# Optimization experiments

Hardware: AMD Instinct MI355X
Metric: run time of the kernel (lower is better)

The kernel has to match this reference:

```python
import jax, jax.numpy as jnp
import numpy as np

N_HEAD = 8
D_HEAD = 64
HIDDEN = 512
T = 2048
BS = 4
SCALE = D_HEAD ** -0.5


def setup_inputs() -> dict:
    key = jax.random.key(0)
    k1, k2, k3 = jax.random.split(key, 3)
    x = jax.random.normal(k1, (BS, T, HIDDEN), dtype=jnp.float32)
    # torch Linear weight is (out,in); we store as (in,out) for x @ W
    W_qkv = jax.random.normal(k2, (HIDDEN, (2 * N_HEAD + 1) * D_HEAD), dtype=jnp.float32) * 0.02
    W_out = jax.random.normal(k3, (D_HEAD, HIDDEN), dtype=jnp.float32) * 0.02
    return {"x": x, "W_qkv": W_qkv, "W_out": W_out}


def reference(x, W_qkv, W_out):
    bs, t, h = x.shape
    qkv = x @ W_qkv  # (bs, t, (2H+1)*d)
    q, k, v = jnp.split(qkv, [N_HEAD * D_HEAD, 2 * N_HEAD * D_HEAD], axis=-1)
    q = q.reshape(bs, t, N_HEAD, D_HEAD)
    k = k.reshape(bs, t, N_HEAD, D_HEAD)
    # v is shared across heads: (bs, t, d)
    score = jnp.einsum("bqhd,bkhd->bhqk", q, k) * SCALE
    causal = jnp.triu(jnp.full((t, t), -jnp.inf, dtype=score.dtype), 1)
    score = score + causal[None, None, :, :]
    prob = jax.nn.softmax(score, axis=-1)  # (bs, H, t, t)
    attn_vec = jnp.einsum("bhqk,bkd->bhqd", prob, v)  # shared V broadcast over heads
    m_attn_vec = jnp.mean(attn_vec, axis=1)  # head-mean: (bs, t, d)
    out = m_attn_vec @ W_out  # (bs, t, hidden)
    return out, attn_vec
```

## Files before the change

kernel.cpp:

```cpp
#include <hip/hip_runtime.h>
#include <hip/hip_bf16.h>

#define NHEAD  8
#define DHEAD  64
#define HIDDEN 512
#define SEQ_T  2048
#define BATCH  4
#define NQKV   1088
#define QPITCH 1152
#define NT     32
#define NROWS  (BATCH * SEQ_T)
#define NBH    (BATCH * NHEAD)
#define QSC    (0.125f * 1.44269504f)

typedef __attribute__((ext_vector_type(8))) short short8;
typedef __attribute__((ext_vector_type(4))) float f32x4;

__device__ __forceinline__ unsigned short f2bf(float f) {
  unsigned int u = __float_as_uint(f);
  u += 0x7FFFu + ((u >> 16) & 1u);
  return (unsigned short)(u >> 16);
}
__device__ __forceinline__ float bf2f(unsigned short u) {
  return __uint_as_float((unsigned int)u << 16);
}

__device__ __forceinline__ void load_lds16(const unsigned short* g, unsigned short* l) {
  __builtin_amdgcn_global_load_lds((const __attribute__((address_space(1))) void*)g,
                                   (__attribute__((address_space(3))) void*)l, 16, 0, 0);
}

__global__ __launch_bounds__(256) void prep(const float* __restrict__ x,
                                            const float* __restrict__ W,
                                            unsigned short* __restrict__ xb,
                                            unsigned short* __restrict__ Wt) {
  const int bx = blockIdx.x;
  const int tid = threadIdx.x;
  if (bx < 2048) {
    const size_t i0 = ((size_t)bx * 256 + tid) * 8;
    float4 a = *(const float4*)(x + i0);
    float4 b = *(const float4*)(x + i0 + 4);
    ushort4 u0, u1;
    u0.x = f2bf(a.x); u0.y = f2bf(a.y); u0.z = f2bf(a.z); u0.w = f2bf(a.w);
    u1.x = f2bf(b.x); u1.y = f2bf(b.y); u1.z = f2bf(b.z); u1.w = f2bf(b.w);
    *(ushort4*)(xb + i0) = u0;
    *(ushort4*)(xb + i0 + 4) = u1;
    return;
  }
  if (bx >= 2184) {
    const int z = bx - 2184;
    const size_t base = (size_t)NQKV * HIDDEN + ((size_t)z * 256 + tid) * 16;
    uint4 zero = {0u, 0u, 0u, 0u};
    *(uint4*)(Wt + base) = zero;
    *(uint4*)(Wt + base + 8) = zero;
    return;
  }
  const int idx = bx - 2048;
  const int n0 = (idx % 17) * 64;
  const int k0 = (idx / 17) * 64;
  __shared__ float T[64 * 65];
#pragma unroll
  for (int i = 0; i < 4; ++i) {
    int f = tid + i * 256;
    int r = f >> 4;
    int c4 = (f & 15) * 4;
    float4 v = *(const float4*)(W + (size_t)(k0 + r) * NQKV + n0 + c4);
    T[r * 65 + c4 + 0] = v.x;
    T[r * 65 + c4 + 1] = v.y;
    T[r * 65 + c4 + 2] = v.z;
    T[r * 65 + c4 + 3] = v.w;
  }
  __syncthreads();
#pragma unroll
  for (int i = 0; i < 4; ++i) {
    int f = tid + i * 256;
    int n = f >> 4;
    int k4 = (f & 15) * 4;
    ushort4 u;
    u.x = f2bf(T[(k4 + 0) * 65 + n]);
    u.y = f2bf(T[(k4 + 1) * 65 + n]);
    u.z = f2bf(T[(k4 + 2) * 65 + n]);
    u.w = f2bf(T[(k4 + 3) * 65 + n]);
    *(ushort4*)(Wt + (size_t)(n0 + n) * HIDDEN + k0 + k4) = u;
  }
}

__global__ __launch_bounds__(256, 3) void qkv_mfma(const unsigned short* __restrict__ Xb,
                                                   const unsigned short* __restrict__ Wt,
                                                   unsigned short* __restrict__ Y) {
  __shared__ __align__(16) unsigned short As[128 * 64];
  __shared__ __align__(16) unsigned short Bs[128 * 64];
  const int L = blockIdx.x;
  const int slot = L >> 3;
  const int bm = (L & 7) * 8 + (slot & 7);
  const int bn = slot >> 3;
  const int tid = threadIdx.x;
  const int wave = tid >> 6;
  const int lane = tid & 63;
  const int quad = lane >> 4;
  const int l15 = lane & 15;
  const int lrow = lane >> 3;
  const int lchunk = lane & 7;

  const unsigned short* xrow = Xb + (size_t)bm * 128 * HIDDEN;
  const unsigned short* wrow = Wt + (size_t)bn * 128 * HIDDEN;

  f32x4 acc[2][8];
#pragma unroll
  for (int mt = 0; mt < 2; ++mt)
#pragma unroll
    for (int nt = 0; nt < 8; ++nt) acc[mt][nt] = (f32x4){0.f, 0.f, 0.f, 0.f};

  for (int k0 = 0; k0 < HIDDEN; k0 += 64) {
    __syncthreads();
#pragma unroll
    for (int c = 0; c < 4; ++c) {
      int call = wave * 4 + c;
      int m = call * 8 + lrow;
      int clog = lchunk ^ lrow;
      load_lds16(xrow + (size_t)m * HIDDEN + k0 + clog * 8, &As[call * 512]);
      load_lds16(wrow + (size_t)m * HIDDEN + k0 + clog * 8, &Bs[call * 512]);
    }
    __syncthreads();

#pragma unroll
    for (int ks = 0; ks < 2; ++ks) {
      short8 a[2], b[8];
#pragma unroll
      for (int mt = 0; mt < 2; ++mt) {
        int m = wave * 32 + mt * 16 + l15;
        int phys = (ks * 4 + quad) ^ (l15 & 7);
        a[mt] = *(const short8*)&As[m * 64 + phys * 8];
      }
#pragma unroll
      for (int nt = 0; nt < 8; ++nt) {
        int n = nt * 16 + l15;
        int phys = (ks * 4 + quad) ^ (l15 & 7);
        b[nt] = *(const short8*)&Bs[n * 64 + phys * 8];
      }
#pragma unroll
      for (int mt = 0; mt < 2; ++mt)
#pragma unroll
        for (int nt = 0; nt < 8; ++nt)
          acc[mt][nt] = __builtin_amdgcn_mfma_f32_16x16x32_bf16(a[mt], b[nt], acc[mt][nt], 0, 0, 0);
    }
  }

  const float qs = (bn < 4) ? QSC : 1.0f;
#pragma unroll
  for (int mt = 0; mt < 2; ++mt)
#pragma unroll
    for (int r = 0; r < 4; ++r) {
      int row = bm * 128 + wave * 32 + mt * 16 + quad * 4 + r;
#pragma unroll
      for (int nt = 0; nt < 8; ++nt) {
        int col = bn * 128 + nt * 16 + l15;
        Y[(size_t)row * QPITCH + col] = f2bf(acc[mt][nt][r] * qs);
      }
    }
}

__global__ __launch_bounds__(256) void v_transpose(const unsigned short* __restrict__ qkv,
                                                   unsigned short* __restrict__ vt) {
  const int b = blockIdx.x >> 5;
  const int k0 = (blockIdx.x & 31) * 64;
  const int tid = threadIdx.x;
  __shared__ unsigned short Vs[64 * 66];

#pragma unroll
  for (int i = 0; i < 8; ++i) {
    int c = tid + i * 256;
    int row = c >> 5;
    int col2 = c & 31;
    unsigned int v = *(const unsigned int*)(qkv + (size_t)(b * SEQ_T + k0 + row) * QPITCH + 1024 + col2 * 2);
    *(unsigned int*)&Vs[row * 66 + col2 * 2] = v;
  }
  __syncthreads();

#pragma unroll
  for (int i = 0; i < 16; ++i) {
    int f = tid + i * 256;
    int d = f >> 6;
    int n = f & 63;
    int c = (n & 32) | ((n & 4) << 2) | ((n >> 1) & 12) | (n & 3);
    vt[((size_t)b * DHEAD + d) * SEQ_T + k0 + n] = Vs[c * 66 + d];
  }
}

__global__ __launch_bounds__(256, 4) void attn_pass(const unsigned short* __restrict__ qkv,
                                                    const unsigned short* __restrict__ vt,
                                                    unsigned short* __restrict__ pbuf0,
                                                    unsigned short* __restrict__ pbuf1,
                                                    float* __restrict__ lbuf) {
  const int bh = blockIdx.x;
  const int y = blockIdx.y;
  const int qt = 15 - (y >> 1);
  const int kh = y & 1;
  const int b = bh >> 3;
  const int h = bh & 7;
  const int tid = threadIdx.x;
  const int wave = tid >> 6;
  const int lane = tid & 63;
  const int quad = lane >> 4;
  const int l15 = lane & 15;

  __shared__ __align__(16) unsigned short Ks[2][64 * 64];
  __shared__ __align__(16) unsigned short Vts[2][64 * 64];

  const unsigned short* bq = qkv + (size_t)b * SEQ_T * QPITCH;
  const unsigned short* bvt = vt + (size_t)b * DHEAD * SEQ_T;

  const int q0 = qt * 128;
  const int kbeg = kh ? (qt + 1) : 0;
  const int kend = kh ? (2 * qt + 1) : qt;

  short8 aq[2][2];
#pragma unroll
  for (int s = 0; s < 2; ++s) {
    const unsigned short* qp = bq + (size_t)(q0 + s * 64 + wave * 16 + l15) * QPITCH + h * 64 + quad * 8;
    aq[s][0] = *(const short8*)qp;
    aq[s][1] = *(const short8*)(qp + 32);
  }

  f32x4 o[2][4];
#pragma unroll
  for (int s = 0; s < 2; ++s)
#pragma unroll
    for (int t = 0; t < 4; ++t) o[s][t] = (f32x4){0.f, 0.f, 0.f, 0.f};
  float l_part[2] = {0.f, 0.f};

  const int srow = tid >> 3;
  const int sch = (tid & 7) ^ (srow & 7);
  const int ph0 = (quad ^ (l15 & 7)) * 8;

#pragma unroll
  for (int c = 0; c < 2; ++c) {
    load_lds16(bq + (size_t)(kbeg * 64 + c * 32 + srow) * QPITCH + 512 + h * 64 + sch * 8,
               &Ks[0][c * 2048 + wave * 512]);
    load_lds16(bvt + (size_t)(c * 32 + srow) * SEQ_T + kbeg * 64 + sch * 8,
               &Vts[0][c * 2048 + wave * 512]);
  }

  for (int kt = kbeg; kt <= kend; ++kt) {
    const int k0 = kt * 64;
    const int cur = (kt - kbeg) & 1;
    __syncthreads();
    if (kt < kend) {
      const int kn = (kt + 1) * 64;
      const int nxt = cur ^ 1;
#pragma unroll
      for (int c = 0; c < 2; ++c) {
        load_lds16(bq + (size_t)(kn + c * 32 + srow) * QPITCH + 512 + h * 64 + sch * 8,
                   &Ks[nxt][c * 2048 + wave * 512]);
        load_lds16(bvt + (size_t)(c * 32 + srow) * SEQ_T + kn + sch * 8,
                   &Vts[nxt][c * 2048 + wave * 512]);
      }
    }

    const unsigned short* ksb = Ks[cur];
    const unsigned short* vsb = Vts[cur];
    const bool needMask = (k0 + 63) > q0;

    short8 bk[4][2];
#pragma unroll
    for (int t = 0; t < 4; ++t) {
      const unsigned short* kp = &ksb[(l15 + 16 * t) * 64];
      bk[t][0] = *(const short8*)(kp + ph0);
      bk[t][1] = *(const short8*)(kp + (ph0 ^ 32));
    }

    short8 ap[2][2];
#pragma unroll
    for (int s = 0; s < 2; ++s) {
      f32x4 pr[4];
#pragma unroll
      for (int t = 0; t < 4; ++t) {
        f32x4 sv = (f32x4){0.f, 0.f, 0.f, 0.f};
        sv = __builtin_amdgcn_mfma_f32_16x16x32_bf16(bk[t][0], aq[s][0], sv, 0, 0, 0);
        sv = __builtin_amdgcn_mfma_f32_16x16x32_bf16(bk[t][1], aq[s][1], sv, 0, 0, 0);
        pr[t] = sv;
      }
      const int qrow = q0 + s * 64 + wave * 16 + l15;
#pragma unroll
      for (int t = 0; t < 4; ++t)
#pragma unroll
        for (int r = 0; r < 4; ++r) {
          float p = __builtin_amdgcn_exp2f(pr[t][r]);
          if (needMask)
            p = (k0 + 16 * t + 4 * quad + r <= qrow) ? p : 0.f;
          l_part[s] += p;
          pr[t][r] = p;
        }
#pragma unroll
      for (int c = 0; c < 2; ++c) {
        union { unsigned int u[4]; short8 v; } pk;
        pk.u[0] = __builtin_amdgcn_perm(__float_as_uint(pr[2 * c][1]),
                                        __float_as_uint(pr[2 * c][0]), 0x07060302u);
        pk.u[1] = __builtin_amdgcn_perm(__float_as_uint(pr[2 * c][3]),
                                        __float_as_uint(pr[2 * c][2]), 0x07060302u);
        pk.u[2] = __builtin_amdgcn_perm(__float_as_uint(pr[2 * c + 1][1]),
                                        __float_as_uint(pr[2 * c + 1][0]), 0x07060302u);
        pk.u[3] = __builtin_amdgcn_perm(__float_as_uint(pr[2 * c + 1][3]),
                                        __float_as_uint(pr[2 * c + 1][2]), 0x07060302u);
        ap[s][c] = pk.v;
      }
    }

    short8 bv[4][2];
#pragma unroll
    for (int t = 0; t < 4; ++t) {
      const unsigned short* vp = &vsb[(l15 + 16 * t) * 64];
      bv[t][0] = *(const short8*)(vp + ph0);
      bv[t][1] = *(const short8*)(vp + (ph0 ^ 32));
    }

#pragma unroll
    for (int t = 0; t < 4; ++t)
#pragma unroll
      for (int s = 0; s < 2; ++s) {
        o[s][t] = __builtin_amdgcn_mfma_f32_16x16x32_bf16(ap[s][0], bv[t][0], o[s][t], 0, 0, 0);
        o[s][t] = __builtin_amdgcn_mfma_f32_16x16x32_bf16(ap[s][1], bv[t][1], o[s][t], 0, 0, 0);
      }
  }

  unsigned short* pb = kh ? pbuf1 : pbuf0;
#pragma unroll
  for (int s = 0; s < 2; ++s) {
    float l = l_part[s];
    l += __shfl_xor(l, 16);
    l += __shfl_xor(l, 32);
    if (lane < 16)
      lbuf[kh * (NBH * SEQ_T) + bh * SEQ_T + q0 + s * 64 + wave * 16 + l15] = l;
#pragma unroll
    for (int r = 0; r < 4; ++r) {
      const int trow = q0 + s * 64 + wave * 16 + quad * 4 + r;
      const size_t base = ((size_t)bh * SEQ_T + trow) * DHEAD;
#pragma unroll
      for (int t = 0; t < 4; ++t) pb[base + l15 + 16 * t] = f2bf(o[s][t][r]);
    }
  }
}

__global__ __launch_bounds__(256) void out_merge(const unsigned short* __restrict__ pbuf0,
                                                 const unsigned short* __restrict__ pbuf1,
                                                 const float* __restrict__ lbuf,
                                                 const float* __restrict__ Wout,
                                                 float* __restrict__ attnv,
                                                 float* __restrict__ out) {
  const int row0 = blockIdx.x * 16;
  const int tid = threadIdx.x;
  __shared__ float Ms[16][64];

  {
    const int lr = tid >> 4;
    const int d0 = (tid & 15) * 4;
    const int row = row0 + lr;
    const int b = row >> 11;
    const int t = row & 2047;
    float s0 = 0.f, s1 = 0.f, s2 = 0.f, s3 = 0.f;
#pragma unroll
    for (int hh = 0; hh < NHEAD; ++hh) {
      const size_t ridx = (size_t)(b * NHEAD + hh) * SEQ_T + t;
      const float inv = 1.0f / (lbuf[ridx] + lbuf[NBH * SEQ_T + ridx]);
      const size_t idx = ridx * DHEAD + d0;
      ushort4 A = *(const ushort4*)(pbuf0 + idx);
      ushort4 B = *(const ushort4*)(pbuf1 + idx);
      float4 m;
      m.x = (bf2f(A.x) + bf2f(B.x)) * inv;
      m.y = (bf2f(A.y) + bf2f(B.y)) * inv;
      m.z = (bf2f(A.z) + bf2f(B.z)) * inv;
      m.w = (bf2f(A.w) + bf2f(B.w)) * inv;
      *(float4*)(attnv + idx) = m;
      s0 += m.x; s1 += m.y; s2 += m.z; s3 += m.w;
    }
    Ms[lr][d0 + 0] = s0 * 0.125f;
    Ms[lr][d0 + 1] = s1 * 0.125f;
    Ms[lr][d0 + 2] = s2 * 0.125f;
    Ms[lr][d0 + 3] = s3 * 0.125f;
  }
  __syncthreads();

  const int c0 = tid * 2;
  float a0[16], a1[16];
#pragma unroll
  for (int i = 0; i < 16; ++i) { a0[i] = 0.f; a1[i] = 0.f; }

  for (int d = 0; d < 64; ++d) {
    float2 w = *(const float2*)(Wout + (size_t)d * HIDDEN + c0);
#pragma unroll
    for (int lr = 0; lr < 16; ++lr) {
      float m = Ms[lr][d];
      a0[lr] += m * w.x;
      a1[lr] += m * w.y;
    }
  }
#pragma unroll
  for (int lr = 0; lr < 16; ++lr) {
    float2 v = make_float2(a0[lr], a1[lr]);
    *(float2*)(out + (size_t)(row0 + lr) * HIDDEN + c0) = v;
  }
}

extern "C" void kernel_launch(void* const* d_in, const int* in_sizes, int n_in,
                              void* d_out, int out_size, void* d_ws, size_t ws_size,
                              hipStream_t stream) {
  const float* x     = (const float*)d_in[0];
  const float* W_qkv = (const float*)d_in[1];
  const float* W_out = (const float*)d_in[2];

  float* out      = (float*)d_out;
  float* attn_vec = out + (size_t)BATCH * SEQ_T * HIDDEN;

  unsigned short* qkv  = (unsigned short*)d_ws;
  unsigned short* vt   = qkv + (size_t)NROWS * QPITCH;
  unsigned short* xb   = vt + (size_t)BATCH * DHEAD * SEQ_T;
  unsigned short* Wt   = xb + (size_t)NROWS * HIDDEN;
  unsigned short* pbuf0 = Wt + (size_t)QPITCH * HIDDEN;
  unsigned short* pbuf1 = pbuf0 + (size_t)NBH * SEQ_T * DHEAD;
  float*          lbuf  = (float*)(pbuf1 + (size_t)NBH * SEQ_T * DHEAD);

  prep<<<dim3(2048 + 136 + 8), 256, 0, stream>>>(x, W_qkv, xb, Wt);
  qkv_mfma<<<dim3(576), 256, 0, stream>>>(xb, Wt, qkv);
  v_transpose<<<dim3(BATCH * NT), 256, 0, stream>>>(qkv, vt);
  attn_pass<<<dim3(NBH, 32), 256, 0, stream>>>(qkv, vt, pbuf0, pbuf1, lbuf);
  out_merge<<<dim3(512), 256, 0, stream>>>(pbuf0, pbuf1, lbuf, W_out, attn_vec, out);
}
```

Measured before the change: 142.9 us.

## Fuse V transpose into QKV GEMM, MFMA row sums and MFMA output projection

The V transpose now happens in the QKV GEMM epilogue for the V column tile, so the separate v_transpose kernel and its reread of V are gone. In attn_pass, softmax row sums are computed with an MFMA against a ones vector instead of per-lane adds and shuffles, and launch bounds drop from 4 to 3 blocks per SM. The output projection in out_merge uses bf16 MFMA with a pre-transposed bf16 W_out, built by prep, in place of scalar fp32 FMA loops. Together these cut one launch and reduce scalar work, but the projection loses precision and occupancy may fall.

```diff
diff --git a/kernel.cpp b/kernel.cpp
--- a/kernel.cpp
+++ b/kernel.cpp
@@ -32,8 +32,10 @@
 
 __global__ __launch_bounds__(256) void prep(const float* __restrict__ x,
                                             const float* __restrict__ W,
+                                            const float* __restrict__ Wout,
                                             unsigned short* __restrict__ xb,
-                                            unsigned short* __restrict__ Wt) {
+                                            unsigned short* __restrict__ Wt,
+                                            unsigned short* __restrict__ Wob) {
   const int bx = blockIdx.x;
   const int tid = threadIdx.x;
   if (bx < 2048) {
@@ -47,12 +49,41 @@
     *(ushort4*)(xb + i0 + 4) = u1;
     return;
   }
-  if (bx >= 2184) {
+  if (bx >= 2184 && bx < 2192) {
     const int z = bx - 2184;
     const size_t base = (size_t)NQKV * HIDDEN + ((size_t)z * 256 + tid) * 16;
     uint4 zero = {0u, 0u, 0u, 0u};
     *(uint4*)(Wt + base) = zero;
     *(uint4*)(Wt + base + 8) = zero;
+    return;
+  }
+  if (bx >= 2192) {
+    const int n0 = (bx - 2192) * 64;
+    __shared__ float T[64 * 65];
+#pragma unroll
+    for (int i = 0; i < 4; ++i) {
+      int f = tid + i * 256;
+      int r = f >> 4;
+      int c4 = (f & 15) * 4;
+      float4 v = *(const float4*)(Wout + (size_t)r * HIDDEN + n0 + c4);
+      T[r * 65 + c4 + 0] = v.x;
+      T[r * 65 + c4 + 1] = v.y;
+      T[r * 65 + c4 + 2] = v.z;
+      T[r * 65 + c4 + 3] = v.w;
+    }
+    __syncthreads();
+#pragma unroll
+    for (int i = 0; i < 4; ++i) {
+      int f = tid + i * 256;
+      int n = f >> 4;
+      int k4 = (f & 15) * 4;
+      ushort4 u;
+      u.x = f2bf(T[(k4 + 0) * 65 + n]);
+      u.y = f2bf(T[(k4 + 1) * 65 + n]);
+      u.z = f2bf(T[(k4 + 2) * 65 + n]);
+      u.w = f2bf(T[(k4 + 3) * 65 + n]);
+      *(ushort4*)(Wob + (size_t)(n0 + n) * DHEAD + k4) = u;
+    }
     return;
   }
   const int idx = bx - 2048;
@@ -87,9 +118,11 @@
 
 __global__ __launch_bounds__(256, 3) void qkv_mfma(const unsigned short* __restrict__ Xb,
                                                    const unsigned short* __restrict__ Wt,
-                                                   unsigned short* __restrict__ Y) {
-  __shared__ __align__(16) unsigned short As[128 * 64];
-  __shared__ __align__(16) unsigned short Bs[128 * 64];
+                                                   unsigned short* __restrict__ Y,
+                                                   unsigned short* __restrict__ vt) {
+  __shared__ __align__(16) unsigned short SH[2 * 128 * 64];
+  unsigned short* As = SH;
+  unsigned short* Bs = SH + 128 * 64;
   const int L = blockIdx.x;
   const int slot = L >> 3;
   const int bm = (L & 7) * 8 + (slot & 7);
@@ -146,48 +179,48 @@
     }
   }
 
-  const float qs = (bn < 4) ? QSC : 1.0f;
-#pragma unroll
-  for (int mt = 0; mt < 2; ++mt)
-#pragma unroll
-    for (int r = 0; r < 4; ++r) {
-      int row = bm * 128 + wave * 32 + mt * 16 + quad * 4 + r;
-#pragma unroll
-      for (int nt = 0; nt < 8; ++nt) {
-        int col = bn * 128 + nt * 16 + l15;
-        Y[(size_t)row * QPITCH + col] = f2bf(acc[mt][nt][r] * qs);
-      }
-    }
-}
-
-__global__ __launch_bounds__(256) void v_transpose(const unsigned short* __restrict__ qkv,
-                                                   unsigned short* __restrict__ vt) {
-  const int b = blockIdx.x >> 5;
-  const int k0 = (blockIdx.x & 31) * 64;
-  const int tid = threadIdx.x;
-  __shared__ unsigned short Vs[64 * 66];
-
-#pragma unroll
-  for (int i = 0; i < 8; ++i) {
-    int c = tid + i * 256;
-    int row = c >> 5;
-    int col2 = c & 31;
-    unsigned int v = *(const unsigned int*)(qkv + (size_t)(b * SEQ_T + k0 + row) * QPITCH + 1024 + col2 * 2);
-    *(unsigned int*)&Vs[row * 66 + col2 * 2] = v;
-  }
-  __syncthreads();
-
-#pragma unroll
-  for (int i = 0; i < 16; ++i) {
-    int f = tid + i * 256;
-    int d = f >> 6;
-    int n = f & 63;
-    int c = (n & 32) | ((n & 4) << 2) | ((n >> 1) & 12) | (n & 3);
-    vt[((size_t)b * DHEAD + d) * SEQ_T + k0 + n] = Vs[c * 66 + d];
-  }
-}
-
-__global__ __launch_bounds__(256, 4) void attn_pass(const unsigned short* __restrict__ qkv,
+  if (bn != 8) {
+    const float qs = (bn < 4) ? QSC : 1.0f;
+#pragma unroll
+    for (int mt = 0; mt < 2; ++mt)
+#pragma unroll
+      for (int r = 0; r < 4; ++r) {
+        int row = bm * 128 + wave * 32 + mt * 16 + quad * 4 + r;
+#pragma unroll
+        for (int nt = 0; nt < 8; ++nt) {
+          int col = bn * 128 + nt * 16 + l15;
+          Y[(size_t)row * QPITCH + col] = f2bf(acc[mt][nt][r] * qs);
+        }
+      }
+  } else {
+    __syncthreads();
+    unsigned short* Vs = SH;
+#pragma unroll
+    for (int mt = 0; mt < 2; ++mt)
+#pragma unroll
+      for (int nt = 0; nt < 4; ++nt)
+#pragma unroll
+        for (int r = 0; r < 4; ++r) {
+          int lr = wave * 32 + mt * 16 + quad * 4 + r;
+          int d = nt * 16 + l15;
+          Vs[d * 130 + lr] = f2bf(acc[mt][nt][r]);
+        }
+    __syncthreads();
+    const int bb = bm >> 4;
+    const int t0 = (bm & 15) * 128;
+    const int half = lane >> 5;
+    const int np = lane & 31;
+    const int s2 = ((np & 16) << 1) | ((np & 2) << 3) | (np & 12) | ((np & 1) << 1);
+#pragma unroll
+    for (int i = 0; i < 16; ++i) {
+      int d = i * 4 + wave;
+      unsigned int v = *(const unsigned int*)&Vs[d * 130 + half * 64 + s2];
+      *(unsigned int*)&vt[((size_t)bb * DHEAD + d) * SEQ_T + t0 + half * 64 + 2 * np] = v;
+    }
+  }
+}
+
+__global__ __launch_bounds__(256, 3) void attn_pass(const unsigned short* __restrict__ qkv,
                                                     const unsigned short* __restrict__ vt,
                                                     unsigned short* __restrict__ pbuf0,
                                                     unsigned short* __restrict__ pbuf1,
@@ -227,7 +260,9 @@
   for (int s = 0; s < 2; ++s)
 #pragma unroll
     for (int t = 0; t < 4; ++t) o[s][t] = (f32x4){0.f, 0.f, 0.f, 0.f};
-  float l_part[2] = {0.f, 0.f};
+  f32x4 ol[2] = {(f32x4){0.f, 0.f, 0.f, 0.f}, (f32x4){0.f, 0.f, 0.f, 0.f}};
+  const short8 vone = {(short)0x3F80, (short)0x3F80, (short)0x3F80, (short)0x3F80,
+                       (short)0x3F80, (short)0x3F80, (short)0x3F80, (short)0x3F80};
 
   const int srow = tid >> 3;
   const int sch = (tid & 7) ^ (srow & 7);
@@ -288,7 +323,6 @@
           float p = __builtin_amdgcn_exp2f(pr[t][r]);
           if (needMask)
             p = (k0 + 16 * t + 4 * quad + r <= qrow) ? p : 0.f;
-          l_part[s] += p;
           pr[t][r] = p;
         }
 #pragma unroll
@@ -304,6 +338,8 @@
                                         __float_as_uint(pr[2 * c + 1][2]), 0x07060302u);
         ap[s][c] = pk.v;
       }
+      ol[s] = __builtin_amdgcn_mfma_f32_16x16x32_bf16(ap[s][0], vone, ol[s], 0, 0, 0);
+      ol[s] = __builtin_amdgcn_mfma_f32_16x16x32_bf16(ap[s][1], vone, ol[s], 0, 0, 0);
     }
 
     short8 bv[4][2];
@@ -326,14 +362,10 @@
   unsigned short* pb = kh ? pbuf1 : pbuf0;
 #pragma unroll
   for (int s = 0; s < 2; ++s) {
-    float l = l_part[s];
-    l += __shfl_xor(l, 16);
-    l += __shfl_xor(l, 32);
-    if (lane < 16)
-      lbuf[kh * (NBH * SEQ_T) + bh * SEQ_T + q0 + s * 64 + wave * 16 + l15] = l;
 #pragma unroll
     for (int r = 0; r < 4; ++r) {
       const int trow = q0 + s * 64 + wave * 16 + quad * 4 + r;
+      if (l15 == 0) lbuf[kh * (NBH * SEQ_T) + bh * SEQ_T + trow] = ol[s][r];
       const size_t base = ((size_t)bh * SEQ_T + trow) * DHEAD;
 #pragma unroll
       for (int t = 0; t < 4; ++t) pb[base + l15 + 16 * t] = f2bf(o[s][t][r]);
@@ -344,12 +376,12 @@
 __global__ __launch_bounds__(256) void out_merge(const unsigned short* __restrict__ pbuf0,
                                                  const unsigned short* __restrict__ pbuf1,
                                                  const float* __restrict__ lbuf,
-                                                 const float* __restrict__ Wout,
+                                                 const unsigned short* __restrict__ Wob,
                                                  float* __restrict__ attnv,
                                                  float* __restrict__ out) {
   const int row0 = blockIdx.x * 16;
   const int tid = threadIdx.x;
-  __shared__ float Ms[16][64];
+  __shared__ float Ms[16][66];
 
   {
     const int lr = tid >> 4;
@@ -380,24 +412,34 @@
   }
   __syncthreads();
 
-  const int c0 = tid * 2;
-  float a0[16], a1[16];
-#pragma unroll
-  for (int i = 0; i < 16; ++i) { a0[i] = 0.f; a1[i] = 0.f; }
-
-  for (int d = 0; d < 64; ++d) {
-    float2 w = *(const float2*)(Wout + (size_t)d * HIDDEN + c0);
-#pragma unroll
-    for (int lr = 0; lr < 16; ++lr) {
-      float m = Ms[lr][d];
-      a0[lr] += m * w.x;
-      a1[lr] += m * w.y;
-    }
-  }
-#pragma unroll
-  for (int lr = 0; lr < 16; ++lr) {
-    float2 v = make_float2(a0[lr], a1[lr]);
-    *(float2*)(out + (size_t)(row0 + lr) * HIDDEN + c0) = v;
+  const int wv = tid >> 6;
+  const int lane = tid & 63;
+  const int quad = lane >> 4;
+  const int l15 = lane & 15;
+
+  short8 am[2];
+  {
+    union { unsigned short us[16]; short8 v[2]; } u;
+#pragma unroll
+    for (int j = 0; j < 8; ++j) {
+      u.us[j] = f2bf(Ms[l15][quad * 8 + j]);
+      u.us[8 + j] = f2bf(Ms[l15][32 + quad * 8 + j]);
+    }
+    am[0] = u.v[0];
+    am[1] = u.v[1];
+  }
+
+#pragma unroll
+  for (int nt = 0; nt < 8; ++nt) {
+    const int n = wv * 128 + nt * 16 + l15;
+    short8 b0 = *(const short8*)&Wob[(size_t)n * DHEAD + quad * 8];
+    short8 b1 = *(const short8*)&Wob[(size_t)n * DHEAD + 32 + quad * 8];
+    f32x4 c = (f32x4){0.f, 0.f, 0.f, 0.f};
+    c = __builtin_amdgcn_mfma_f32_16x16x32_bf16(am[0], b0, c, 0, 0, 0);
+    c = __builtin_amdgcn_mfma_f32_16x16x32_bf16(am[1], b1, c, 0, 0, 0);
+#pragma unroll
+    for (int r = 0; r < 4; ++r)
+      out[(size_t)(row0 + quad * 4 + r) * HIDDEN + n] = c[r];
   }
 }
 
@@ -418,10 +460,10 @@
   unsigned short* pbuf0 = Wt + (size_t)QPITCH * HIDDEN;
   unsigned short* pbuf1 = pbuf0 + (size_t)NBH * SEQ_T * DHEAD;
   float*          lbuf  = (float*)(pbuf1 + (size_t)NBH * SEQ_T * DHEAD);
-
-  prep<<<dim3(2048 + 136 + 8), 256, 0, stream>>>(x, W_qkv, xb, Wt);
-  qkv_mfma<<<dim3(576), 256, 0, stream>>>(xb, Wt, qkv);
-  v_transpose<<<dim3(BATCH * NT), 256, 0, stream>>>(qkv, vt);
+  unsigned short* Wob   = (unsigned short*)(lbuf + 2 * NBH * SEQ_T);
+
+  prep<<<dim3(2048 + 136 + 8 + 8), 256, 0, stream>>>(x, W_qkv, W_out, xb, Wt, Wob);
+  qkv_mfma<<<dim3(576), 256, 0, stream>>>(xb, Wt, qkv, vt);
   attn_pass<<<dim3(NBH, 32), 256, 0, stream>>>(qkv, vt, pbuf0, pbuf1, lbuf);
-  out_merge<<<dim3(512), 256, 0, stream>>>(pbuf0, pbuf1, lbuf, W_out, attn_vec, out);
-}
+  out_merge<<<dim3(512), 256, 0, stream>>>(pbuf0, pbuf1, lbuf, Wob, attn_vec, out);
+}
```

After: 130.1 us. 1.1x faster.
